# Optimization experiments

Measured on AMD Instinct MI355X. Metric: run time of the kernel, lower is better.

## Reference

```python
import jax, jax.numpy as jnp
import numpy as np

SIZE = 65536
MAX_EDGES = 16777216  # n_edges = min(0.1*SIZE^2, MAX_EDGES) = MAX_EDGES, so all edges active


def setup_inputs() -> dict:
    key = jax.random.key(0)
    k1, k2, k3, k4 = jax.random.split(key, 4)
    x = jax.random.normal(k1, (SIZE,), dtype=jnp.float32)
    edge_weights = jax.random.normal(k2, (MAX_EDGES,), dtype=jnp.float32) * (2.0 / SIZE) ** 0.5
    bias = jnp.zeros((SIZE,), dtype=jnp.float32)
    src = jax.random.randint(k3, (MAX_EDGES,), 0, SIZE, dtype=jnp.int64 if jax.config.jax_enable_x64 else jnp.int32)
    dst = jax.random.randint(k4, (MAX_EDGES,), 0, SIZE, dtype=jnp.int64 if jax.config.jax_enable_x64 else jnp.int32)
    return {"x": x, "edge_weights": edge_weights, "bias": bias, "src": src, "dst": dst}


def reference(x, edge_weights, bias, src, dst):
    # gather -> elementwise multiply -> scatter_add -> + bias
    weighted = x[src] * edge_weights                    # [E]
    out = jax.ops.segment_sum(weighted, dst, num_segments=SIZE)  # [size]
    return out + bias
```

## Files before the change

### kernel.cpp

```cpp
#include <hip/hip_runtime.h>


#define NNODES  65536
#define NEDGES  16777216
#define RANGES  2
#define BINS    (NNODES / RANGES)
#define THREADS 1024
#define NCOPIES 128
#define GROUPS  16
#define CPG     (NCOPIES / GROUPS)

__global__ __launch_bounds__(THREADS, 4) void hist_kernel(
    const float* __restrict__ x,
    const float* __restrict__ w,
    const int*   __restrict__ src,
    const int*   __restrict__ dst,
    float*       __restrict__ ws,
    int B)
{
    extern __shared__ float h[];

    const int b  = blockIdx.x;
    const int r  = b & (RANGES - 1);
    const int c  = b >> 1;
    const int lo = r * BINS;

    for (int i = threadIdx.x; i < BINS; i += THREADS) h[i] = 0.0f;
    __syncthreads();

    const int4*   src4 = (const int4*)src;
    const int4*   dst4 = (const int4*)dst;
    const float4* wgt4 = (const float4*)w;

    const int n8 = NEDGES / 8;
    for (int g = c * THREADS + (int)threadIdx.x; g < n8; g += B * THREADS) {
        int4   sa = src4[2 * g], sb = src4[2 * g + 1];
        int4   da = dst4[2 * g], db = dst4[2 * g + 1];
        float4 wa = wgt4[2 * g], wb = wgt4[2 * g + 1];

        int      s[8]  = { sa.x, sa.y, sa.z, sa.w, sb.x, sb.y, sb.z, sb.w };
        unsigned bin[8] = {
            (unsigned)(da.x - lo), (unsigned)(da.y - lo),
            (unsigned)(da.z - lo), (unsigned)(da.w - lo),
            (unsigned)(db.x - lo), (unsigned)(db.y - lo),
            (unsigned)(db.z - lo), (unsigned)(db.w - lo) };
        float    wv[8] = { wa.x, wa.y, wa.z, wa.w, wb.x, wb.y, wb.z, wb.w };

        float v[8];
        #pragma unroll
        for (int k = 0; k < 8; ++k) {
            v[k] = 0.0f;
            if (bin[k] < (unsigned)BINS) v[k] = x[s[k]] * wv[k];
        }
        #pragma unroll
        for (int k = 0; k < 8; ++k) {
            if (bin[k] < (unsigned)BINS) atomicAdd(&h[bin[k]], v[k]);
        }
    }
    __syncthreads();

    float* outc = ws + (size_t)c * NNODES + lo;
    for (int i = threadIdx.x; i < BINS; i += THREADS) outc[i] = h[i];
}

__global__ __launch_bounds__(256) void reduceA_kernel(float* __restrict__ ws)
{
    const int NB = NNODES / (256 * 4);
    int g  = blockIdx.x / NB;
    int jb = blockIdx.x % NB;
    int i4 = jb * 256 + (int)threadIdx.x;

    float4* w4 = (float4*)ws;
    const int stride4 = NNODES / 4;

    float4 acc = w4[(size_t)(g * CPG) * stride4 + i4];
    #pragma unroll
    for (int cc = 1; cc < CPG; ++cc) {
        float4 t = w4[(size_t)(g * CPG + cc) * stride4 + i4];
        acc.x += t.x; acc.y += t.y; acc.z += t.z; acc.w += t.w;
    }
    w4[(size_t)(g * CPG) * stride4 + i4] = acc;
}

__global__ __launch_bounds__(256) void reduceB_kernel(
    const float* __restrict__ ws,
    const float* __restrict__ bias,
    float*       __restrict__ out)
{
    int i4 = blockIdx.x * 256 + (int)threadIdx.x;
    const float4* w4 = (const float4*)ws;
    const int stride4 = NNODES / 4;

    float4 acc = ((const float4*)bias)[i4];
    #pragma unroll
    for (int g = 0; g < GROUPS; ++g) {
        float4 t = w4[(size_t)(g * CPG) * stride4 + i4];
        acc.x += t.x; acc.y += t.y; acc.z += t.z; acc.w += t.w;
    }
    ((float4*)out)[i4] = acc;
}

__global__ __launch_bounds__(256) void reduce_generic_kernel(
    const float* __restrict__ ws,
    const float* __restrict__ bias,
    float*       __restrict__ out,
    int B)
{
    int i = blockIdx.x * 256 + (int)threadIdx.x;
    float acc = bias[i];
    for (int cc = 0; cc < B; ++cc) acc += ws[(size_t)cc * NNODES + i];
    out[i] = acc;
}

__global__ __launch_bounds__(256) void init_out_kernel(
    const float* __restrict__ bias, float* __restrict__ out)
{
    int i = blockIdx.x * blockDim.x + threadIdx.x;
    if (i < NNODES) out[i] = bias[i];
}

__global__ __launch_bounds__(256) void edge_atomic_kernel(
    const float* __restrict__ x, const float* __restrict__ w,
    const int* __restrict__ src, const int* __restrict__ dst,
    float* __restrict__ out)
{
    const int n4 = NEDGES / 4;
    int tid = blockIdx.x * blockDim.x + threadIdx.x;
    int stride = gridDim.x * blockDim.x;
    for (int i = tid; i < n4; i += stride) {
        int4 s = ((const int4*)src)[i];
        int4 d = ((const int4*)dst)[i];
        float4 ww = ((const float4*)w)[i];
        atomicAdd(&out[d.x], x[s.x] * ww.x);
        atomicAdd(&out[d.y], x[s.y] * ww.y);
        atomicAdd(&out[d.z], x[s.z] * ww.z);
        atomicAdd(&out[d.w], x[s.w] * ww.w);
    }
}

extern "C" void kernel_launch(void* const* d_in, const int* in_sizes, int n_in,
                              void* d_out, int out_size, void* d_ws, size_t ws_size,
                              hipStream_t stream) {
    const float* x    = (const float*)d_in[0];
    const float* w    = (const float*)d_in[1];
    const float* bias = (const float*)d_in[2];
    const int*   src  = (const int*)d_in[3];
    const int*   dst  = (const int*)d_in[4];
    float* out = (float*)d_out;
    float* ws  = (float*)d_ws;

    size_t copies = ws_size / ((size_t)NNODES * sizeof(float));
    int B = (int)(copies < NCOPIES ? copies : NCOPIES);

    if (B >= 1) {
        hist_kernel<<<B * RANGES, THREADS, BINS * sizeof(float), stream>>>(
            x, w, src, dst, ws, B);
        if (B == NCOPIES) {
            reduceA_kernel<<<GROUPS * (NNODES / 1024), 256, 0, stream>>>(ws);
            reduceB_kernel<<<NNODES / 1024, 256, 0, stream>>>(ws, bias, out);
        } else {
            reduce_generic_kernel<<<NNODES / 256, 256, 0, stream>>>(ws, bias, out, B);
        }
    } else {
        init_out_kernel<<<NNODES / 256, 256, 0, stream>>>(bias, out);
        edge_atomic_kernel<<<4096, 256, 0, stream>>>(x, w, src, dst, out);
    }
}
```

Before: 273.5 us.

## Software-pipeline edge loads and gathers across iterations, remap block-to-range ordering

The histogram loop is restructured into a three-stage software pipeline: edge indices and weights are loaded two iterations ahead and x gathers run one iteration ahead, overlapping with the shared-memory atomics for the current batch. The aim is to hide global memory latency behind the LDS atomic work. Gathers are now unconditional, so every edge's x value is fetched even when it falls outside the block's bin range, which adds gather traffic. The block index mapping also changes so that consecutive blocks share a range in groups of eight, which alters which blocks read the same edge chunks concurrently and may affect L2 reuse. Register pressure rises because of the extra in-flight state.

```diff
diff --git a/kernel.cpp b/kernel.cpp
--- a/kernel.cpp
+++ b/kernel.cpp
@@ -10,6 +10,51 @@
 #define GROUPS  16
 #define CPG     (NCOPIES / GROUPS)
 
+struct E8 { int4 sa, sb, da, db; float4 wa, wb; };
+struct V8 { float v0, v1, v2, v3, v4, v5, v6, v7; };
+
+__device__ __forceinline__ E8 load8(const int4* __restrict__ s4,
+                                    const int4* __restrict__ d4,
+                                    const float4* __restrict__ w4, int g) {
+    E8 e;
+    e.sa = s4[2 * g];  e.sb = s4[2 * g + 1];
+    e.da = d4[2 * g];  e.db = d4[2 * g + 1];
+    e.wa = w4[2 * g];  e.wb = w4[2 * g + 1];
+    return e;
+}
+
+__device__ __forceinline__ V8 gather8(const float* __restrict__ x, const E8& e) {
+    V8 r;
+    r.v0 = x[e.sa.x] * e.wa.x;
+    r.v1 = x[e.sa.y] * e.wa.y;
+    r.v2 = x[e.sa.z] * e.wa.z;
+    r.v3 = x[e.sa.w] * e.wa.w;
+    r.v4 = x[e.sb.x] * e.wb.x;
+    r.v5 = x[e.sb.y] * e.wb.y;
+    r.v6 = x[e.sb.z] * e.wb.z;
+    r.v7 = x[e.sb.w] * e.wb.w;
+    return r;
+}
+
+__device__ __forceinline__ void atom8(float* h, int lo, const E8& e, const V8& r) {
+    unsigned b0 = (unsigned)(e.da.x - lo);
+    unsigned b1 = (unsigned)(e.da.y - lo);
+    unsigned b2 = (unsigned)(e.da.z - lo);
+    unsigned b3 = (unsigned)(e.da.w - lo);
+    unsigned b4 = (unsigned)(e.db.x - lo);
+    unsigned b5 = (unsigned)(e.db.y - lo);
+    unsigned b6 = (unsigned)(e.db.z - lo);
+    unsigned b7 = (unsigned)(e.db.w - lo);
+    if (b0 < (unsigned)BINS) atomicAdd(&h[b0], r.v0);
+    if (b1 < (unsigned)BINS) atomicAdd(&h[b1], r.v1);
+    if (b2 < (unsigned)BINS) atomicAdd(&h[b2], r.v2);
+    if (b3 < (unsigned)BINS) atomicAdd(&h[b3], r.v3);
+    if (b4 < (unsigned)BINS) atomicAdd(&h[b4], r.v4);
+    if (b5 < (unsigned)BINS) atomicAdd(&h[b5], r.v5);
+    if (b6 < (unsigned)BINS) atomicAdd(&h[b6], r.v6);
+    if (b7 < (unsigned)BINS) atomicAdd(&h[b7], r.v7);
+}
+
 __global__ __launch_bounds__(THREADS, 4) void hist_kernel(
     const float* __restrict__ x,
     const float* __restrict__ w,
@@ -21,8 +66,8 @@
     extern __shared__ float h[];
 
     const int b  = blockIdx.x;
-    const int r  = b & (RANGES - 1);
-    const int c  = b >> 1;
+    const int r  = (b >> 3) & (RANGES - 1);
+    const int c  = (b & 7) | ((b >> 4) << 3);
     const int lo = r * BINS;
 
     for (int i = threadIdx.x; i < BINS; i += THREADS) h[i] = 0.0f;
@@ -32,31 +77,33 @@
     const int4*   dst4 = (const int4*)dst;
     const float4* wgt4 = (const float4*)w;
 
-    const int n8 = NEDGES / 8;
-    for (int g = c * THREADS + (int)threadIdx.x; g < n8; g += B * THREADS) {
-        int4   sa = src4[2 * g], sb = src4[2 * g + 1];
-        int4   da = dst4[2 * g], db = dst4[2 * g + 1];
-        float4 wa = wgt4[2 * g], wb = wgt4[2 * g + 1];
-
-        int      s[8]  = { sa.x, sa.y, sa.z, sa.w, sb.x, sb.y, sb.z, sb.w };
-        unsigned bin[8] = {
-            (unsigned)(da.x - lo), (unsigned)(da.y - lo),
-            (unsigned)(da.z - lo), (unsigned)(da.w - lo),
-            (unsigned)(db.x - lo), (unsigned)(db.y - lo),
-            (unsigned)(db.z - lo), (unsigned)(db.w - lo) };
-        float    wv[8] = { wa.x, wa.y, wa.z, wa.w, wb.x, wb.y, wb.z, wb.w };
-
-        float v[8];
-        #pragma unroll
-        for (int k = 0; k < 8; ++k) {
-            v[k] = 0.0f;
-            if (bin[k] < (unsigned)BINS) v[k] = x[s[k]] * wv[k];
+    const int n8     = NEDGES / 8;
+    const int stride = B * THREADS;
+    const int g0     = c * THREADS + (int)threadIdx.x;
+
+    if ((n8 % stride) == 0 && (n8 / stride) >= 2) {
+        const int niter = n8 / stride;
+        E8 e0 = load8(src4, dst4, wgt4, g0);
+        V8 r0 = gather8(x, e0);
+        E8 e1 = load8(src4, dst4, wgt4, g0 + stride);
+        int g2 = g0 + 2 * stride;
+        for (int it = 0; it < niter - 2; ++it, g2 += stride) {
+            E8 e2 = load8(src4, dst4, wgt4, g2);
+            V8 r1 = gather8(x, e1);
+            atom8(h, lo, e0, r0);
+            e0 = e1; r0 = r1; e1 = e2;
         }
-        #pragma unroll
-        for (int k = 0; k < 8; ++k) {
-            if (bin[k] < (unsigned)BINS) atomicAdd(&h[bin[k]], v[k]);
+        V8 r1 = gather8(x, e1);
+        atom8(h, lo, e0, r0);
+        atom8(h, lo, e1, r1);
+    } else {
+        for (int g = g0; g < n8; g += stride) {
+            E8 e = load8(src4, dst4, wgt4, g);
+            V8 v = gather8(x, e);
+            atom8(h, lo, e, v);
         }
     }
+
     __syncthreads();
 
     float* outc = ws + (size_t)c * NNODES + lo;
```

New measurement: 320.7 us. +17.2%, slower.
